# Kernel tuning notes

Measured on AMD Instinct MI355X. Metric: run time of the kernel, lower is better.

Reference implementation:

```python
import jax, jax.numpy as jnp
import numpy as np

N = 50000   # num nodes
E = 500000  # num edges
D = 128     # latent_size


def _mlp_params(key, d_in, d_hid, d_out):
    k1, k2 = jax.random.split(key)
    return (jax.random.normal(k1, (d_in, d_hid), jnp.float32) * 0.05,
            jnp.zeros((d_hid,), jnp.float32),
            jax.random.normal(k2, (d_hid, d_out), jnp.float32) * 0.05,
            jnp.zeros((d_out,), jnp.float32))


def setup_inputs() -> dict:
    key = jax.random.key(0)
    ks = jax.random.split(key, 16)
    inp = {
        'edge_index': jax.random.randint(ks[0], (2, E), 0, N, dtype=jnp.int32),
        'edge_attr': jax.random.randint(ks[1], (E, 1), 0, 3, dtype=jnp.int32) - 1,   # {-1,0,1}; -1 => virtual edge
        'node_type': jax.random.randint(ks[2], (N, 2), 0, 3, dtype=jnp.int32) - 1,  # last col == -1 => global node
        'senders_pos': jax.random.normal(ks[3], (E, 3), jnp.float32),
        'receivers_pos': jax.random.normal(ks[4], (E, 3), jnp.float32),
        'vector_a': jax.random.normal(ks[5], (E, 3), jnp.float32),
        'vector_b': jax.random.normal(ks[6], (E, 3), jnp.float32),
        'vector_c': jax.random.normal(ks[7], (E, 3), jnp.float32),
        'interaction_latent': jax.random.normal(ks[8], (E, D), jnp.float32),
        'w_nodes': jax.random.uniform(ks[9], (N, 1), jnp.float32) + 0.1,  # positive masses
    }
    for name, kk, d_out in (('i1', ks[10], 3), ('i2', ks[11], 3), ('fs', ks[12], 1), ('dx', ks[13], 3)):
        W1, b1, W2, b2 = _mlp_params(kk, D, D, d_out)
        inp[name + '_W1'], inp[name + '_b1'], inp[name + '_W2'], inp[name + '_b2'] = W1, b1, W2, b2
    return inp


def _mlp(x, W1, b1, W2, b2):
    return jax.nn.relu(x @ W1 + b1) @ W2 + b2


def _remove_mean(t, mask, idx):
    # subtract per-node mean of masked edges, only on masked entries
    m = mask[:, None].astype(t.dtype)
    s = jax.ops.segment_sum(t * m, idx, num_segments=N)       # [N,3]
    c = jax.ops.segment_sum(m, idx, num_segments=N)           # [N,1]
    mean = s / jnp.maximum(c, 1.0)
    return t - mean[idx] * m


def reference(edge_index, edge_attr, senders_pos, receivers_pos, vector_a, vector_b,
              vector_c, interaction_latent, w_nodes, node_type,
              i1_W1, i1_b1, i1_W2, i1_b2,
              i2_W1, i2_b1, i2_W2, i2_b2,
              fs_W1, fs_b1, fs_W2, fs_b2,
              dx_W1, dx_b1, dx_W2, dx_b2):
    senders, receivers = edge_index[0], edge_index[1]
    coeff_f = _mlp(interaction_latent, i1_W1, i1_b1, i1_W2, i1_b2)   # [E,3]
    coeff_a = _mlp(interaction_latent, i2_W1, i2_b1, i2_W2, i2_b2)   # [E,3]
    lambda_ij = _mlp(interaction_latent, fs_W1, fs_b1, fs_W2, fs_b2) # [E,1]
    coeff_dx = _mlp(interaction_latent, dx_W1, dx_b1, dx_W2, dx_b2)  # [E,3]

    fij = coeff_f[:, 0:1] * vector_a + coeff_f[:, 1:2] * vector_b + coeff_f[:, 2:3] * vector_c
    aij = coeff_a[:, 0:1] * vector_a + coeff_a[:, 1:2] * vector_b + coeff_a[:, 2:3] * vector_c
    dxij = coeff_dx[:, 0:1] * vector_a + coeff_dx[:, 1:2] * vector_b + coeff_dx[:, 2:3] * vector_c

    is_global = node_type[:, -1] == -1            # [N]
    is_virtual = (edge_attr == -1).reshape(-1)    # [E]

    mask_in = is_virtual & is_global[receivers]
    fij = _remove_mean(fij, mask_in, receivers)
    aij = _remove_mean(aij, mask_in, receivers)
    dxij = _remove_mean(dxij, mask_in, receivers)

    mask_out = is_virtual & is_global[senders]
    fij = _remove_mean(fij, mask_out, senders)
    aij = _remove_mean(aij, mask_out, senders)
    dxij = _remove_mean(dxij, mask_out, senders)

    w_s, w_r = w_nodes[senders], w_nodes[receivers]            # [E,1]
    r0ij = (w_s * senders_pos + w_r * receivers_pos) / (w_s + w_r)
    lever_arm = receivers_pos - r0ij
    torque_contribution = jnp.cross(lever_arm, fij * lambda_ij)
    tauij = aij - torque_contribution
    return (fij, tauij, dxij)
```

## Files before the change

### kernel.cpp

```cpp
#include <hip/hip_runtime.h>
#include <hip/hip_bf16.h>

#define NN 50000
#define NE 500000
#define DD 128

typedef float  f32x4 __attribute__((ext_vector_type(4)));
typedef short  s16x8 __attribute__((ext_vector_type(8)));

struct MlpPtrs { const float* W1; const float* b1; const float* W2; const float* b2; int dout; int obase; };
struct MlpArgs { MlpPtrs m[4]; };

__device__ __forceinline__ unsigned short f2bf(float f) {
    unsigned int u = __builtin_bit_cast(unsigned int, f);
    u += 0x7fffu + ((u >> 16) & 1u);
    return (unsigned short)(u >> 16);
}

__global__ void prep_w1t_kernel(const float* __restrict__ W1a, const float* __restrict__ W1b,
                                const float* __restrict__ W1c, const float* __restrict__ W1d,
                                unsigned short* __restrict__ w1t)
{
    int idx = blockIdx.x * blockDim.x + threadIdx.x;
    if (idx >= 4 * DD * DD) return;
    int m = idx >> 14, r = idx & 16383;
    int j = r >> 7, k = r & 127;
    const float* W1 = (m == 0) ? W1a : (m == 1) ? W1b : (m == 2) ? W1c : W1d;
    w1t[idx] = f2bf(W1[k * DD + j]);
}

__global__ __launch_bounds__(256) void mlp_mfma_kernel(
    const float* __restrict__ latent, const unsigned short* __restrict__ w1t,
    const float* __restrict__ va, const float* __restrict__ vb, const float* __restrict__ vc,
    float* __restrict__ out, float* __restrict__ lam_ws, MlpArgs args)
{
    __shared__ unsigned short Ws[DD * 136];
    __shared__ float W2s[DD * 3];
    __shared__ float Cf[4][32][10];

    const int t = threadIdx.x;
    const int wave = t >> 6, l = t & 63;
    const int lg = l >> 4, lr = l & 15;
    const int e0 = blockIdx.x * 128 + wave * 32;

    s16x8 a[2][4];
    #pragma unroll
    for (int mf = 0; mf < 2; ++mf) {
        int e = e0 + mf * 16 + lr; if (e >= NE) e = NE - 1;
        const float* src = latent + (size_t)e * DD + lg * 8;
        #pragma unroll
        for (int kc = 0; kc < 4; ++kc) {
            float4 x0 = *(const float4*)(src + kc * 32);
            float4 x1 = *(const float4*)(src + kc * 32 + 4);
            s16x8 v;
            v[0] = (short)f2bf(x0.x); v[1] = (short)f2bf(x0.y);
            v[2] = (short)f2bf(x0.z); v[3] = (short)f2bf(x0.w);
            v[4] = (short)f2bf(x1.x); v[5] = (short)f2bf(x1.y);
            v[6] = (short)f2bf(x1.z); v[7] = (short)f2bf(x1.w);
            a[mf][kc] = v;
        }
    }

    for (int m = 0; m < 4; ++m) {
        const MlpPtrs P = args.m[m];
        __syncthreads();
        {
            const uint4* src = (const uint4*)(w1t + m * DD * DD);
            #pragma unroll
            for (int i = 0; i < 8; ++i) {
                int idx16 = t + i * 256;
                uint4 vv = src[idx16];
                int j = idx16 >> 4, k = (idx16 & 15) * 8;
                *(uint4*)&Ws[j * 136 + k] = vv;
            }
        }
        for (int i = t; i < DD * P.dout; i += 256) W2s[i] = P.W2[i];
        __syncthreads();

        f32x4 acc[2][8];
        #pragma unroll
        for (int mf = 0; mf < 2; ++mf)
            #pragma unroll
            for (int nf = 0; nf < 8; ++nf) {
                f32x4 z = {0.f, 0.f, 0.f, 0.f};
                acc[mf][nf] = z;
            }
        #pragma unroll
        for (int nf = 0; nf < 8; ++nf) {
            #pragma unroll
            for (int kc = 0; kc < 4; ++kc) {
                s16x8 b = *(const s16x8*)&Ws[(lr + 16 * nf) * 136 + lg * 8 + kc * 32];
                acc[0][nf] = __builtin_amdgcn_mfma_f32_16x16x32_bf16(a[0][kc], b, acc[0][nf], 0, 0, 0);
                acc[1][nf] = __builtin_amdgcn_mfma_f32_16x16x32_bf16(a[1][kc], b, acc[1][nf], 0, 0, 0);
            }
        }
        #pragma unroll
        for (int nf = 0; nf < 8; ++nf) {
            float bv = P.b1[16 * nf + lr];
            #pragma unroll
            for (int mf = 0; mf < 2; ++mf)
                #pragma unroll
                for (int r = 0; r < 4; ++r)
                    acc[mf][nf][r] = fmaxf(acc[mf][nf][r] + bv, 0.f);
        }
        for (int o = 0; o < P.dout; ++o) {
            float w2v[8];
            #pragma unroll
            for (int nf = 0; nf < 8; ++nf) w2v[nf] = W2s[(16 * nf + lr) * P.dout + o];
            float p[2][4];
            #pragma unroll
            for (int mf = 0; mf < 2; ++mf)
                #pragma unroll
                for (int r = 0; r < 4; ++r) {
                    float s = 0.f;
                    #pragma unroll
                    for (int nf = 0; nf < 8; ++nf) s = fmaf(acc[mf][nf][r], w2v[nf], s);
                    s += __shfl_xor(s, 8);
                    s += __shfl_xor(s, 4);
                    s += __shfl_xor(s, 2);
                    s += __shfl_xor(s, 1);
                    p[mf][r] = s;
                }
            if (lr == 0) {
                float b2v = P.b2[o];
                #pragma unroll
                for (int mf = 0; mf < 2; ++mf)
                    #pragma unroll
                    for (int r = 0; r < 4; ++r)
                        Cf[wave][mf * 16 + lg * 4 + r][P.obase + o] = p[mf][r] + b2v;
            }
        }
    }
    __syncthreads();

    if (l < 32) {
        const int e = e0 + l;
        if (e < NE) {
            float c[10];
            #pragma unroll
            for (int q = 0; q < 10; ++q) c[q] = Cf[wave][l][q];
            const float ax = va[(size_t)e*3+0], ay = va[(size_t)e*3+1], az = va[(size_t)e*3+2];
            const float bx = vb[(size_t)e*3+0], by = vb[(size_t)e*3+1], bz = vb[(size_t)e*3+2];
            const float cx = vc[(size_t)e*3+0], cy = vc[(size_t)e*3+1], cz = vc[(size_t)e*3+2];
            const size_t o0 = (size_t)e * 3;
            const size_t o1 = (size_t)NE * 3 + o0;
            const size_t o2 = (size_t)2 * NE * 3 + o0;
            out[o0+0] = c[0]*ax + c[1]*bx + c[2]*cx;
            out[o0+1] = c[0]*ay + c[1]*by + c[2]*cy;
            out[o0+2] = c[0]*az + c[1]*bz + c[2]*cz;
            out[o1+0] = c[3]*ax + c[4]*bx + c[5]*cx;
            out[o1+1] = c[3]*ay + c[4]*by + c[5]*cy;
            out[o1+2] = c[3]*az + c[4]*bz + c[5]*cz;
            out[o2+0] = c[7]*ax + c[8]*bx + c[9]*cx;
            out[o2+1] = c[7]*ay + c[8]*by + c[9]*cy;
            out[o2+2] = c[7]*az + c[8]*bz + c[9]*cz;
            lam_ws[e] = c[6];
        }
    }
}

__global__ void zero_kernel(float* __restrict__ p, int n)
{
    int i = blockIdx.x * blockDim.x + threadIdx.x;
    if (i < n) p[i] = 0.0f;
}

__global__ void seg_sum_kernel(const int* __restrict__ idx, const int* __restrict__ edge_attr,
                               const int* __restrict__ node_type, const float* __restrict__ out,
                               float* __restrict__ sums, float* __restrict__ cnt)
{
    int e = blockIdx.x * blockDim.x + threadIdx.x;
    if (e >= NE) return;
    if (edge_attr[e] != -1) return;
    const int n = idx[e];
    if (node_type[2 * n + 1] != -1) return;
    atomicAdd(&cnt[n], 1.0f);
    #pragma unroll
    for (int tns = 0; tns < 3; ++tns)
        #pragma unroll
        for (int c2 = 0; c2 < 3; ++c2)
            atomicAdd(&sums[(size_t)tns * 3 * NN + (size_t)n * 3 + c2],
                      out[(size_t)tns * NE * 3 + (size_t)e * 3 + c2]);
}

__global__ void apply_mean_kernel(const int* __restrict__ idx, const int* __restrict__ edge_attr,
                                  const int* __restrict__ node_type, float* __restrict__ out,
                                  const float* __restrict__ sums, const float* __restrict__ cnt)
{
    int e = blockIdx.x * blockDim.x + threadIdx.x;
    if (e >= NE) return;
    if (edge_attr[e] != -1) return;
    const int n = idx[e];
    if (node_type[2 * n + 1] != -1) return;
    const float ic = 1.0f / fmaxf(cnt[n], 1.0f);
    #pragma unroll
    for (int tns = 0; tns < 3; ++tns)
        #pragma unroll
        for (int c2 = 0; c2 < 3; ++c2)
            out[(size_t)tns * NE * 3 + (size_t)e * 3 + c2] -=
                sums[(size_t)tns * 3 * NN + (size_t)n * 3 + c2] * ic;
}

__global__ void finalize_kernel(const int* __restrict__ senders, const int* __restrict__ receivers,
                                const float* __restrict__ sp, const float* __restrict__ rp,
                                const float* __restrict__ wn, const float* __restrict__ lam,
                                float* __restrict__ out)
{
    int e = blockIdx.x * blockDim.x + threadIdx.x;
    if (e >= NE) return;
    const int s = senders[e], r = receivers[e];
    const float wsv = wn[s], wrv = wn[r];
    const float inv = 1.0f / (wsv + wrv);
    const size_t b = (size_t)e * 3;
    const float spx = sp[b+0], spy = sp[b+1], spz = sp[b+2];
    const float rpx = rp[b+0], rpy = rp[b+1], rpz = rp[b+2];
    const float lx = rpx - (wsv * spx + wrv * rpx) * inv;
    const float ly = rpy - (wsv * spy + wrv * rpy) * inv;
    const float lz = rpz - (wsv * spz + wrv * rpz) * inv;
    const float lv = lam[e];
    const float gx = out[b+0] * lv, gy = out[b+1] * lv, gz = out[b+2] * lv;
    const size_t tb = (size_t)NE * 3 + b;
    const float tx = out[tb+0] - (ly * gz - lz * gy);
    const float ty = out[tb+1] - (lz * gx - lx * gz);
    const float tz = out[tb+2] - (lx * gy - ly * gx);
    out[tb+0] = tx; out[tb+1] = ty; out[tb+2] = tz;
}

extern "C" void kernel_launch(void* const* d_in, const int* in_sizes, int n_in,
                              void* d_out, int out_size, void* d_ws, size_t ws_size,
                              hipStream_t stream)
{
    (void)in_sizes; (void)n_in; (void)out_size; (void)ws_size;

    const int* edge_index    = (const int*)d_in[0];
    const int* edge_attr     = (const int*)d_in[1];
    const int* node_type     = (const int*)d_in[2];
    const float* senders_pos = (const float*)d_in[3];
    const float* recv_pos    = (const float*)d_in[4];
    const float* vector_a    = (const float*)d_in[5];
    const float* vector_b    = (const float*)d_in[6];
    const float* vector_c    = (const float*)d_in[7];
    const float* latent      = (const float*)d_in[8];
    const float* w_nodes     = (const float*)d_in[9];

    MlpArgs ma;
    const int douts[4] = {3, 3, 1, 3};
    const int obase[4] = {0, 3, 6, 7};
    for (int i = 0; i < 4; ++i) {
        ma.m[i].W1 = (const float*)d_in[10 + i * 4 + 0];
        ma.m[i].b1 = (const float*)d_in[10 + i * 4 + 1];
        ma.m[i].W2 = (const float*)d_in[10 + i * 4 + 2];
        ma.m[i].b2 = (const float*)d_in[10 + i * 4 + 3];
        ma.m[i].dout = douts[i];
        ma.m[i].obase = obase[i];
    }

    float* out = (float*)d_out;
    float* lam    = (float*)d_ws;
    float* segbuf = lam + NE;
    float* sIn    = segbuf;
    float* cIn    = sIn + 9 * NN;
    float* sOut   = cIn + NN;
    float* cOut   = sOut + 9 * NN;
    unsigned short* w1t = (unsigned short*)(cOut + NN);

    const int* senders   = edge_index;
    const int* receivers = edge_index + NE;

    hipLaunchKernelGGL(prep_w1t_kernel, dim3((4 * DD * DD + 255) / 256), dim3(256), 0, stream,
                       ma.m[0].W1, ma.m[1].W1, ma.m[2].W1, ma.m[3].W1, w1t);
    hipLaunchKernelGGL(zero_kernel, dim3((20 * NN + 255) / 256), dim3(256), 0, stream,
                       segbuf, 20 * NN);
    hipLaunchKernelGGL(mlp_mfma_kernel, dim3((NE + 127) / 128), dim3(256), 0, stream,
                       latent, w1t, vector_a, vector_b, vector_c, out, lam, ma);
    dim3 gE((NE + 255) / 256);
    hipLaunchKernelGGL(seg_sum_kernel,    gE, dim3(256), 0, stream, receivers, edge_attr, node_type, out, sIn, cIn);
    hipLaunchKernelGGL(apply_mean_kernel, gE, dim3(256), 0, stream, receivers, edge_attr, node_type, out, sIn, cIn);
    hipLaunchKernelGGL(seg_sum_kernel,    gE, dim3(256), 0, stream, senders, edge_attr, node_type, out, sOut, cOut);
    hipLaunchKernelGGL(apply_mean_kernel, gE, dim3(256), 0, stream, senders, edge_attr, node_type, out, sOut, cOut);
    hipLaunchKernelGGL(finalize_kernel,   gE, dim3(256), 0, stream, senders, receivers, senders_pos, recv_pos, w_nodes, lam, out);
}
```

Baseline: 285.4 us.

## Fuse receiver mean-apply with sender segment-sum, and sender apply with finalize

The separate receiver apply-mean, sender segment-sum, sender apply-mean and finalize kernels are merged into two kernels. The first subtracts the receiver mean and, in the same pass, accumulates the sender sums from the updated values in registers. The second applies the sender mean and computes the torque directly from register values. This removes two launches and several full passes over the edge output buffers. The price is more divergent control flow per thread.

```diff
diff --git a/kernel.cpp b/kernel.cpp
--- a/kernel.cpp
+++ b/kernel.cpp
@@ -183,47 +183,86 @@
                       out[(size_t)tns * NE * 3 + (size_t)e * 3 + c2]);
 }
 
-__global__ void apply_mean_kernel(const int* __restrict__ idx, const int* __restrict__ edge_attr,
-                                  const int* __restrict__ node_type, float* __restrict__ out,
-                                  const float* __restrict__ sums, const float* __restrict__ cnt)
+__global__ void apply_r_sum_s_kernel(const int* __restrict__ senders, const int* __restrict__ receivers,
+                                     const int* __restrict__ edge_attr, const int* __restrict__ node_type,
+                                     float* __restrict__ out,
+                                     const float* __restrict__ sIn, const float* __restrict__ cIn,
+                                     float* __restrict__ sOut, float* __restrict__ cOut)
 {
     int e = blockIdx.x * blockDim.x + threadIdx.x;
     if (e >= NE) return;
     if (edge_attr[e] != -1) return;
-    const int n = idx[e];
-    if (node_type[2 * n + 1] != -1) return;
-    const float ic = 1.0f / fmaxf(cnt[n], 1.0f);
+    const int r = receivers[e], s = senders[e];
+    const bool mr = (node_type[2 * r + 1] == -1);
+    const bool ms = (node_type[2 * s + 1] == -1);
+    if (!mr && !ms) return;
+    float v[9];
     #pragma unroll
     for (int tns = 0; tns < 3; ++tns)
         #pragma unroll
         for (int c2 = 0; c2 < 3; ++c2)
-            out[(size_t)tns * NE * 3 + (size_t)e * 3 + c2] -=
-                sums[(size_t)tns * 3 * NN + (size_t)n * 3 + c2] * ic;
-}
-
-__global__ void finalize_kernel(const int* __restrict__ senders, const int* __restrict__ receivers,
-                                const float* __restrict__ sp, const float* __restrict__ rp,
-                                const float* __restrict__ wn, const float* __restrict__ lam,
-                                float* __restrict__ out)
+            v[tns * 3 + c2] = out[(size_t)tns * NE * 3 + (size_t)e * 3 + c2];
+    if (mr) {
+        const float ic = 1.0f / fmaxf(cIn[r], 1.0f);
+        #pragma unroll
+        for (int tns = 0; tns < 3; ++tns)
+            #pragma unroll
+            for (int c2 = 0; c2 < 3; ++c2) {
+                v[tns * 3 + c2] -= sIn[(size_t)tns * 3 * NN + (size_t)r * 3 + c2] * ic;
+                out[(size_t)tns * NE * 3 + (size_t)e * 3 + c2] = v[tns * 3 + c2];
+            }
+    }
+    if (ms) {
+        atomicAdd(&cOut[s], 1.0f);
+        #pragma unroll
+        for (int tns = 0; tns < 3; ++tns)
+            #pragma unroll
+            for (int c2 = 0; c2 < 3; ++c2)
+                atomicAdd(&sOut[(size_t)tns * 3 * NN + (size_t)s * 3 + c2], v[tns * 3 + c2]);
+    }
+}
+
+__global__ void apply_finalize_kernel(const int* __restrict__ senders, const int* __restrict__ receivers,
+                                      const int* __restrict__ edge_attr, const int* __restrict__ node_type,
+                                      const float* __restrict__ sp, const float* __restrict__ rp,
+                                      const float* __restrict__ wn, const float* __restrict__ lam,
+                                      const float* __restrict__ sums, const float* __restrict__ cnt,
+                                      float* __restrict__ out)
 {
     int e = blockIdx.x * blockDim.x + threadIdx.x;
     if (e >= NE) return;
     const int s = senders[e], r = receivers[e];
+    const size_t b = (size_t)e * 3;
+    const size_t tb = (size_t)NE * 3 + b;
+    const size_t db = (size_t)2 * NE * 3 + b;
+    float fx = out[b+0], fy = out[b+1], fz = out[b+2];
+    float axx = out[tb+0], ayy = out[tb+1], azz = out[tb+2];
+    const bool masked = (edge_attr[e] == -1) && (node_type[2 * s + 1] == -1);
+    if (masked) {
+        const float ic = 1.0f / fmaxf(cnt[s], 1.0f);
+        fx -= sums[(size_t)0 * 3 * NN + (size_t)s * 3 + 0] * ic;
+        fy -= sums[(size_t)0 * 3 * NN + (size_t)s * 3 + 1] * ic;
+        fz -= sums[(size_t)0 * 3 * NN + (size_t)s * 3 + 2] * ic;
+        axx -= sums[(size_t)1 * 3 * NN + (size_t)s * 3 + 0] * ic;
+        ayy -= sums[(size_t)1 * 3 * NN + (size_t)s * 3 + 1] * ic;
+        azz -= sums[(size_t)1 * 3 * NN + (size_t)s * 3 + 2] * ic;
+        out[b+0] = fx; out[b+1] = fy; out[b+2] = fz;
+        out[db+0] -= sums[(size_t)2 * 3 * NN + (size_t)s * 3 + 0] * ic;
+        out[db+1] -= sums[(size_t)2 * 3 * NN + (size_t)s * 3 + 1] * ic;
+        out[db+2] -= sums[(size_t)2 * 3 * NN + (size_t)s * 3 + 2] * ic;
+    }
     const float wsv = wn[s], wrv = wn[r];
     const float inv = 1.0f / (wsv + wrv);
-    const size_t b = (size_t)e * 3;
     const float spx = sp[b+0], spy = sp[b+1], spz = sp[b+2];
     const float rpx = rp[b+0], rpy = rp[b+1], rpz = rp[b+2];
     const float lx = rpx - (wsv * spx + wrv * rpx) * inv;
     const float ly = rpy - (wsv * spy + wrv * rpy) * inv;
     const float lz = rpz - (wsv * spz + wrv * rpz) * inv;
     const float lv = lam[e];
-    const float gx = out[b+0] * lv, gy = out[b+1] * lv, gz = out[b+2] * lv;
-    const size_t tb = (size_t)NE * 3 + b;
-    const float tx = out[tb+0] - (ly * gz - lz * gy);
-    const float ty = out[tb+1] - (lz * gx - lx * gz);
-    const float tz = out[tb+2] - (lx * gy - ly * gx);
-    out[tb+0] = tx; out[tb+1] = ty; out[tb+2] = tz;
+    const float gx = fx * lv, gy = fy * lv, gz = fz * lv;
+    out[tb+0] = axx - (ly * gz - lz * gy);
+    out[tb+1] = ayy - (lz * gx - lx * gz);
+    out[tb+2] = azz - (lx * gy - ly * gx);
 }
 
 extern "C" void kernel_launch(void* const* d_in, const int* in_sizes, int n_in,
@@ -274,9 +313,9 @@
     hipLaunchKernelGGL(mlp_mfma_kernel, dim3((NE + 127) / 128), dim3(256), 0, stream,
                        latent, w1t, vector_a, vector_b, vector_c, out, lam, ma);
     dim3 gE((NE + 255) / 256);
-    hipLaunchKernelGGL(seg_sum_kernel,    gE, dim3(256), 0, stream, receivers, edge_attr, node_type, out, sIn, cIn);
-    hipLaunchKernelGGL(apply_mean_kernel, gE, dim3(256), 0, stream, receivers, edge_attr, node_type, out, sIn, cIn);
-    hipLaunchKernelGGL(seg_sum_kernel,    gE, dim3(256), 0, stream, senders, edge_attr, node_type, out, sOut, cOut);
-    hipLaunchKernelGGL(apply_mean_kernel, gE, dim3(256), 0, stream, senders, edge_attr, node_type, out, sOut, cOut);
-    hipLaunchKernelGGL(finalize_kernel,   gE, dim3(256), 0, stream, senders, receivers, senders_pos, recv_pos, w_nodes, lam, out);
-}
+    hipLaunchKernelGGL(seg_sum_kernel,       gE, dim3(256), 0, stream, receivers, edge_attr, node_type, out, sIn, cIn);
+    hipLaunchKernelGGL(apply_r_sum_s_kernel, gE, dim3(256), 0, stream, senders, receivers, edge_attr, node_type,
+                       out, sIn, cIn, sOut, cOut);
+    hipLaunchKernelGGL(apply_finalize_kernel, gE, dim3(256), 0, stream, senders, receivers, edge_attr, node_type,
+                       senders_pos, recv_pos, w_nodes, lam, sOut, cOut, out);
+}
```

Result: no change. 280.7 us (-1.7%).
